# Kernel tuning notes

Hardware: AMD Instinct MI355X
Metric: run time of the kernel (lower is better)

The kernel has to match this reference:

```python
import jax, jax.numpy as jnp
import numpy as np

N_NODES = 50000
N_EDGES = 800000
IN_DIM = 128
HEADS = 4
CH = 64
NEG_SLOPE = 0.2


def _gat_conv(x, src, dst, W, a_src, a_dst, bias):
    """PyG-style GATConv (self-loops already appended to src/dst).
    x: [N, F_in], W: [F_in, H*C], a_src/a_dst: [H, C], bias: [H*C]."""
    n = x.shape[0]
    h = (x @ W).reshape(n, HEADS, CH)                      # [N, H, C]
    alpha_s = (h * a_src).sum(-1)                          # [N, H]
    alpha_d = (h * a_dst).sum(-1)                          # [N, H]
    e = jax.nn.leaky_relu(alpha_s[src] + alpha_d[dst], NEG_SLOPE)  # [E, H]
    m = jax.ops.segment_max(e, dst, num_segments=n)        # segment softmax over dst
    e = jnp.exp(e - m[dst])
    denom = jax.ops.segment_sum(e, dst, num_segments=n)
    alpha = e / (denom[dst] + 1e-16)                       # [E, H]
    out = jax.ops.segment_sum(h[src] * alpha[:, :, None], dst, num_segments=n)
    return out.reshape(n, HEADS * CH) + bias               # concat=True


def setup_inputs() -> dict:
    key = jax.random.key(0)
    ks = jax.random.split(key, 10)
    x = jax.random.normal(ks[0], (N_NODES, IN_DIM), dtype=jnp.float32)
    edge_index = jax.random.randint(ks[1], (2, N_EDGES), 0, N_NODES, dtype=jnp.int64)
    s1 = 1.0 / np.sqrt(IN_DIM)
    s2 = 1.0 / np.sqrt(HEADS * CH)
    return {
        "x": x,
        "edge_index": edge_index,
        "W1": jax.random.normal(ks[2], (IN_DIM, HEADS * CH), dtype=jnp.float32) * s1,
        "a_src1": jax.random.normal(ks[3], (HEADS, CH), dtype=jnp.float32) * s1,
        "a_dst1": jax.random.normal(ks[4], (HEADS, CH), dtype=jnp.float32) * s1,
        "b1": jnp.zeros((HEADS * CH,), dtype=jnp.float32),
        "W2": jax.random.normal(ks[5], (HEADS * CH, HEADS * CH), dtype=jnp.float32) * s2,
        "a_src2": jax.random.normal(ks[6], (HEADS, CH), dtype=jnp.float32) * s2,
        "a_dst2": jax.random.normal(ks[7], (HEADS, CH), dtype=jnp.float32) * s2,
        "b2": jnp.zeros((HEADS * CH,), dtype=jnp.float32),
        "fc_w": jax.random.normal(ks[8], (HEADS * CH, 1), dtype=jnp.float32) * s2,
        "fc_b": jnp.zeros((1,), dtype=jnp.float32),
    }


def reference(x, edge_index, W1, a_src1, a_dst1, b1, W2, a_src2, a_dst2, b2, fc_w, fc_b):
    n = x.shape[0]
    loop = jnp.arange(n, dtype=edge_index.dtype)           # PyG GATConv adds self-loops
    src = jnp.concatenate([edge_index[0], loop])
    dst = jnp.concatenate([edge_index[1], loop])
    h = jax.nn.elu(_gat_conv(x, src, dst, W1, a_src1, a_dst1, b1))
    h = jax.nn.elu(_gat_conv(h, src, dst, W2, a_src2, a_dst2, b2))
    return jax.nn.sigmoid(h @ fc_w + fc_b)                 # [N, 1]
```

## Files before the change

### kernel.cpp

```cpp
#include <hip/hip_runtime.h>
#include <hip/hip_bf16.h>

#define N_NODES 50000
#define N_EDGES 800000
#define NCHUNK 256
#define EPC 3125
#define NBUCKET 196
#define SCAN_N 50176
#define SCAN_BLOCKS 196

typedef __attribute__((ext_vector_type(8))) short bf16x8;
typedef __attribute__((ext_vector_type(4))) float f32x4;
typedef __attribute__((ext_vector_type(2))) float f32x2;
typedef unsigned short ushort_t;

__device__ __forceinline__ float bf2f(unsigned short u) {
    union { unsigned u32; float f; } v; v.u32 = (unsigned)u << 16; return v.f;
}
__device__ __forceinline__ unsigned short f2bf(float f) {
    __hip_bfloat16 h = __float2bfloat16(f);
    return *reinterpret_cast<unsigned short*>(&h);
}
__device__ __forceinline__ f32x2 bfpair(unsigned u) {
    union { unsigned a; float f; } lo, hi;
    lo.a = u << 16;
    hi.a = u & 0xFFFF0000u;
    f32x2 r; r.x = lo.f; r.y = hi.f; return r;
}
__device__ __forceinline__ void pkfma(f32x2& d, f32x2 a, f32x2 b) {
    asm("v_pk_fma_f32 %0, %1, %2, %0" : "+v"(d) : "v"(a), "v"(b));
}
__device__ __forceinline__ void gload16(const void* src, void* lds) {
    __builtin_amdgcn_global_load_lds(
        (const __attribute__((address_space(1))) unsigned int*)src,
        (__attribute__((address_space(3))) unsigned int*)lds, 16, 0, 0);
}

__device__ __forceinline__ int detect_is32_block(const unsigned* __restrict__ w,
                                                 int* s_is32, int tid) {
    if (tid == 0) {
        unsigned o = 0;
#pragma unroll
        for (int k = 1; k < 32; k += 2) o |= w[k];
        *s_is32 = (o != 0u);
    }
    __syncthreads();
    return *s_is32;
}

__device__ __forceinline__ int edge_elem(const unsigned* __restrict__ w, int is32, long long idx) {
    return is32 ? (int)w[idx] : (int)w[2 * idx];
}

#define CONV_BLOCKS 6250
#define PREP_W_BLOCKS (CONV_BLOCKS + 128 + 256)
__global__ void __launch_bounds__(256) prep_kernel(const float* __restrict__ x,
                                                   ushort_t* __restrict__ xbf,
                                                   const float* __restrict__ W1,
                                                   ushort_t* __restrict__ W1t,
                                                   const float* __restrict__ W2,
                                                   ushort_t* __restrict__ W2t,
                                                   const unsigned* __restrict__ ew,
                                                   int* __restrict__ chunkHist,
                                                   int* __restrict__ dhist,
                                                   int* __restrict__ dcur) {
    int b = blockIdx.x, t = threadIdx.x;
    if (b < CONV_BLOCKS) {
        if (b == 0 && t < 64) { dhist[t] = 0; dcur[t] = 0; }
        int i = b * 256 + t;
        float4 v = ((const float4*)x)[i];
        ushort4 o;
        o.x = f2bf(v.x); o.y = f2bf(v.y); o.z = f2bf(v.z); o.w = f2bf(v.w);
        ((ushort4*)xbf)[i] = o;
    } else if (b < CONV_BLOCKS + 128) {
        int id = (b - CONV_BLOCKS) * 256 + t;
        int n = id >> 7, k = id & 127;
        W1t[id] = f2bf(W1[k * 256 + n]);
    } else if (b < CONV_BLOCKS + 128 + 256) {
        int id = (b - CONV_BLOCKS - 128) * 256 + t;
        int n = id >> 8, k = id & 255;
        W2t[id] = f2bf(W2[k * 256 + n]);
    } else {
        __shared__ int s_is32;
        __shared__ int hist[NBUCKET];
        int c = b - PREP_W_BLOCKS;
        int is32 = detect_is32_block(ew, &s_is32, t);
        for (int k = t; k < NBUCKET; k += 256) hist[k] = 0;
        __syncthreads();
        long long e0 = (long long)c * EPC;
        for (int k = t; k < EPC; k += 256) {
            int d = edge_elem(ew, is32, (long long)N_EDGES + e0 + k);
            atomicAdd(&hist[d >> 8], 1);
        }
        __syncthreads();
        for (int k = t; k < NBUCKET; k += 256)
            chunkHist[k * NCHUNK + c] = hist[k];
    }
}

__global__ void __launch_bounds__(256) scan1_kernel(const int* __restrict__ in,
                                                    int* __restrict__ excl, int* __restrict__ bsum) {
    __shared__ int s[256];
    int b = blockIdx.x, t = threadIdx.x, i = b * 256 + t;
    int v = in[i];
    s[t] = v;
    __syncthreads();
    for (int off = 1; off < 256; off <<= 1) {
        int y = (t >= off) ? s[t - off] : 0;
        __syncthreads();
        s[t] += y;
        __syncthreads();
    }
    excl[i] = s[t] - v;
    if (t == 255) bsum[b] = s[255];
}

__global__ void __launch_bounds__(256) scan3_kernel(const int* __restrict__ bsum,
                                                    int* __restrict__ excl) {
    __shared__ int sboff;
    int b = blockIdx.x, t = threadIdx.x;
    if (t < 64) {
        int add = 0;
        for (int k = t; k < b; k += 64) add += bsum[k];
#pragma unroll
        for (int off = 32; off; off >>= 1) add += __shfl_down(add, off, 64);
        if (t == 0) sboff = add;
    }
    __syncthreads();
    excl[b * 256 + t] += sboff;
}

__global__ void __launch_bounds__(256) bucket_scatter_kernel(const unsigned* __restrict__ ew,
                                                             const int* __restrict__ chunkOff,
                                                             unsigned* __restrict__ ebuf) {
    __shared__ int s_is32;
    __shared__ int cur[NBUCKET];
    int t = threadIdx.x, b = blockIdx.x;
    int is32 = detect_is32_block(ew, &s_is32, t);
    for (int k = t; k < NBUCKET; k += 256) cur[k] = chunkOff[k * NCHUNK + b];
    __syncthreads();
    long long e0 = (long long)b * EPC;
    for (int k = t; k < EPC; k += 256) {
        long long e = e0 + k;
        unsigned s = (unsigned)edge_elem(ew, is32, e);
        int d = edge_elem(ew, is32, (long long)N_EDGES + e);
        int pos = atomicAdd(&cur[d >> 8], 1);
        ebuf[pos] = s | ((unsigned)d << 16);
    }
}

__global__ void __launch_bounds__(256) bucket_sort_kernel(const unsigned* __restrict__ ebuf,
                                                          const int* __restrict__ chunkOff,
                                                          unsigned* __restrict__ edge_csr,
                                                          int* __restrict__ row_ptr,
                                                          int* __restrict__ dhist) {
    __shared__ int cnt[256];
    __shared__ int s[256];
    __shared__ int dh[64];
    int b = blockIdx.x, t = threadIdx.x;
    int start = chunkOff[b * NCHUNK];
    int end = (b + 1 < NBUCKET) ? chunkOff[(b + 1) * NCHUNK] : N_EDGES;
    cnt[t] = 0;
    if (t < 64) dh[t] = 0;
    __syncthreads();
    for (int e = start + t; e < end; e += 256) {
        int d = (int)(ebuf[e] >> 16);
        atomicAdd(&cnt[d & 255], 1);
    }
    __syncthreads();
    int node = b * 256 + t;
    int mydeg = cnt[t];
    if (node < N_NODES) atomicAdd(&dh[mydeg < 63 ? mydeg : 63], 1);
    s[t] = mydeg;
    __syncthreads();
    for (int off = 1; off < 256; off <<= 1) {
        int y = (t >= off) ? s[t - off] : 0;
        __syncthreads();
        s[t] += y;
        __syncthreads();
    }
    int excl = s[t] - mydeg;
    if (node <= N_NODES) row_ptr[node] = start + excl;
    cnt[t] = start + excl;
    __syncthreads();
    for (int e = start + t; e < end; e += 256) {
        unsigned pk = ebuf[e];
        int pos = atomicAdd(&cnt[(pk >> 16) & 255], 1);
        edge_csr[pos] = pk;
    }
    if (t < 64 && dh[t]) atomicAdd(&dhist[t], dh[t]);
}

__global__ void __launch_bounds__(256) dscatter_kernel(const int* __restrict__ row_ptr,
                                                       const int* __restrict__ dhist,
                                                       int* __restrict__ dcur,
                                                       int* __restrict__ perm) {
    __shared__ int lh[64], lbase[64], sbase[64];
    int t = threadIdx.x, i = blockIdx.x * 256 + t;
    if (t < 64) {
        int v = dhist[t];
        int sum = v;
#pragma unroll
        for (int off = 1; off < 64; off <<= 1) {
            int y = __shfl_up(sum, off, 64);
            if (t >= off) sum += y;
        }
        sbase[t] = sum - v;
        lh[t] = 0;
    }
    __syncthreads();
    int deg = 0;
    if (i < N_NODES) {
        deg = row_ptr[i + 1] - row_ptr[i];
        if (deg > 63) deg = 63;
        atomicAdd(&lh[deg], 1);
    }
    __syncthreads();
    if (t < 64) {
        lbase[t] = lh[t] ? (sbase[t] + atomicAdd(&dcur[t], lh[t])) : 0;
        lh[t] = 0;
    }
    __syncthreads();
    if (i < N_NODES) {
        int rank = atomicAdd(&lh[deg], 1);
        perm[lbase[deg] + rank] = i;
    }
}

template <int K>
__global__ void __launch_bounds__(256) mfma_gemm_kernel(const ushort_t* __restrict__ A,
                                                        const ushort_t* __restrict__ Wt,
                                                        void* __restrict__ Cv, int M,
                                                        const float* __restrict__ a_src,
                                                        const float* __restrict__ a_dst,
                                                        float* __restrict__ alpha_s,
                                                        float* __restrict__ alpha_d) {
    constexpr int CPR = K / 8;
    constexpr int NT = K / 64;
    __shared__ ushort_t Bs[64 * K];
    __shared__ ushort_t As[2][64 * 64];
    __shared__ float ps[64][2], pd[64][2];

    int tid = threadIdx.x;
    int wave = tid >> 6, lane = tid & 63;
    int l15 = lane & 15, l4 = lane >> 4;
    int wr = wave >> 1, wc = wave & 1;
    int colblock = blockIdx.x;
    int rowblock = blockIdx.y;

    for (int base = 0; base < 64 * CPR; base += 256) {
        int p = base + wave * 64 + lane;
        int row = p / CPR;
        int cs = p % CPR;
        int c = cs ^ (row & 7);
        const ushort_t* src = Wt + (long long)(colblock * 64 + row) * K + c * 8;
        void* dst = ((char*)Bs) + (base + wave * 64) * 16;
        gload16(src, dst);
    }
    {
        int r = lane >> 3, cs = lane & 7;
        int c = cs ^ r;
#pragma unroll
        for (int q = 0; q < 2; ++q) {
            int lrow = wave * 16 + q * 8;
            int grow = rowblock * 64 + lrow + r;
            if (grow >= M) grow = M - 1;
            const ushort_t* src = A + (long long)grow * K + c * 8;
            void* dst = ((char*)&As[0][0]) + lrow * 128;
            gload16(src, dst);
        }
    }
    __syncthreads();

    f32x4 acc[2][2] = {};
#pragma unroll
    for (int t = 0; t < NT; ++t) {
        if (t + 1 < NT) {
            int r = lane >> 3, cs = lane & 7;
            int c = cs ^ r;
#pragma unroll
            for (int q = 0; q < 2; ++q) {
                int lrow = wave * 16 + q * 8;
                int grow = rowblock * 64 + lrow + r;
                if (grow >= M) grow = M - 1;
                const ushort_t* src = A + (long long)grow * K + (t + 1) * 64 + c * 8;
                void* dst = ((char*)&As[(t + 1) & 1][0]) + lrow * 128;
                gload16(src, dst);
            }
        }
        const ushort_t* At = &As[t & 1][0];
#pragma unroll
        for (int w = 0; w < 2; ++w) {
            bf16x8 a[2], b[2];
#pragma unroll
            for (int mi = 0; mi < 2; ++mi) {
                int row = wr * 32 + mi * 16 + l15;
                int slot = (w * 4 + l4) ^ (l15 & 7);
                a[mi] = *(const bf16x8*)&At[row * 64 + slot * 8];
            }
#pragma unroll
            for (int ni = 0; ni < 2; ++ni) {
                int brow = wc * 32 + ni * 16 + l15;
                int slot = (t * 8 + w * 4 + l4) ^ (l15 & 7);
                b[ni] = *(const bf16x8*)&Bs[brow * CPR * 8 + slot * 8];
            }
#pragma unroll
            for (int mi = 0; mi < 2; ++mi)
#pragma unroll
                for (int ni = 0; ni < 2; ++ni)
                    acc[mi][ni] = __builtin_amdgcn_mfma_f32_16x16x32_bf16(a[mi], b[ni],
                                                                          acc[mi][ni], 0, 0, 0);
        }
        __syncthreads();
    }

    {
        float as0 = a_src[colblock * 64 + wc * 32 + l15];
        float as1 = a_src[colblock * 64 + wc * 32 + 16 + l15];
        float ad0 = a_dst[colblock * 64 + wc * 32 + l15];
        float ad1 = a_dst[colblock * 64 + wc * 32 + 16 + l15];
#pragma unroll
        for (int mi = 0; mi < 2; ++mi)
#pragma unroll
            for (int q = 0; q < 4; ++q) {
                float sv = acc[mi][0][q] * as0 + acc[mi][1][q] * as1;
                float dv = acc[mi][0][q] * ad0 + acc[mi][1][q] * ad1;
#pragma unroll
                for (int w = 1; w < 16; w <<= 1) {
                    sv += __shfl_xor(sv, w, 64);
                    dv += __shfl_xor(dv, w, 64);
                }
                if (l15 == 0) {
                    int row = wr * 32 + mi * 16 + l4 * 4 + q;
                    ps[row][wc] = sv;
                    pd[row][wc] = dv;
                }
            }
    }

    ushort_t* ep = ((ushort_t*)&As[0][0]) + wave * 1280;
#pragma unroll
    for (int mi = 0; mi < 2; ++mi)
#pragma unroll
        for (int ni = 0; ni < 2; ++ni)
#pragma unroll
            for (int q = 0; q < 4; ++q) {
                int row = mi * 16 + l4 * 4 + q;
                int col = ni * 16 + l15;
                ep[row * 40 + col] = f2bf(acc[mi][ni][q]);
            }
    __syncthreads();
#pragma unroll
    for (int j = 0; j < 2; ++j) {
        int p = lane * 2 + j;
        int row = p >> 2, seg = p & 3;
        uint4 v = *(const uint4*)&ep[row * 40 + seg * 8];
        int grow = rowblock * 64 + wr * 32 + row;
        int gcol = colblock * 64 + wc * 32 + seg * 8;
        if (grow < M) {
            f32x2 f01 = bfpair(v.x), f23 = bfpair(v.y);
            f32x2 f45 = bfpair(v.z), f67 = bfpair(v.w);
            int d0 = 0, d1 = 0;
            d0 = __builtin_amdgcn_cvt_pk_fp8_f32(f01.x, f01.y, d0, false);
            d0 = __builtin_amdgcn_cvt_pk_fp8_f32(f23.x, f23.y, d0, true);
            d1 = __builtin_amdgcn_cvt_pk_fp8_f32(f45.x, f45.y, d1, false);
            d1 = __builtin_amdgcn_cvt_pk_fp8_f32(f67.x, f67.y, d1, true);
            uint2 o; o.x = (unsigned)d0; o.y = (unsigned)d1;
            *(uint2*)((char*)Cv + (long long)grow * 256 + gcol) = o;
        }
    }
    if (tid < 64) {
        int ga = rowblock * 64 + tid;
        if (ga < M) {
            alpha_s[ga * 4 + colblock] = ps[tid][0] + ps[tid][1];
            alpha_d[ga * 4 + colblock] = pd[tid][0] + pd[tid][1];
        }
    }
}

template <int U>
__device__ __forceinline__ void agg_batch(int p, const unsigned* __restrict__ edge_csr,
                                          const float* __restrict__ alpha_s,
                                          const char* __restrict__ gb, unsigned loff,
                                          int l15, int hd, float ad, float& wsum,
                                          f32x2& acc01, f32x2& acc23) {
    int j[U]; unsigned hh[U];
#pragma unroll
    for (int u = 0; u < U; ++u) j[u] = (int)(edge_csr[p + u] & 0xFFFFu);
#pragma unroll
    for (int u = 0; u < U; ++u)
        hh[u] = *(const unsigned*)(gb + (((unsigned)j[u] << 8) | loff));
    int myj = (int)(edge_csr[p + (l15 & (U - 1))] & 0xFFFFu);
    float e = alpha_s[myj * 4 + hd] + ad;
    e = e > 0.f ? e : 0.2f * e;
    float wt_mine = __expf(e);
    int sbase = hd << 4;
#pragma unroll
    for (int u = 0; u < U; ++u) {
        float wt = __shfl(wt_mine, sbase | u, 64);
        wsum += wt;
        f32x2 wp; wp.x = wt; wp.y = wt;
        pkfma(acc01, wp, __builtin_amdgcn_cvt_pk_f32_fp8(hh[u], false));
        pkfma(acc23, wp, __builtin_amdgcn_cvt_pk_f32_fp8(hh[u], true));
    }
}

template <int LAYER>
__global__ void __launch_bounds__(256) aggregate_kernel(
    const void* __restrict__ gv, const float* __restrict__ alpha_s,
    const float* __restrict__ alpha_d, const int* __restrict__ row_ptr,
    const unsigned* __restrict__ edge_csr, const int* __restrict__ perm,
    const float* __restrict__ bias, ushort_t* __restrict__ out_bf,
    const float* __restrict__ fc_w, const float* __restrict__ fc_b,
    float* __restrict__ final_out) {
    int wave = threadIdx.x >> 6;
    int lane = threadIdx.x & 63;
    int i = __builtin_amdgcn_readfirstlane(perm[blockIdx.x * 4 + wave]);
    int hd = lane >> 4;
    int l15 = lane & 15;
    const char* gb = (const char*)gv;
    unsigned loff = (unsigned)(lane << 2);

    float ad = alpha_d[i * 4 + hd];
    float e0 = alpha_s[i * 4 + hd] + ad;
    e0 = e0 > 0.f ? e0 : 0.2f * e0;
    float w0 = __expf(e0);
    f32x2 acc01 = {0.f, 0.f}, acc23 = {0.f, 0.f};
    {
        unsigned sv = *(const unsigned*)(gb + (((unsigned)i << 8) | loff));
        f32x2 wp0; wp0.x = w0; wp0.y = w0;
        pkfma(acc01, wp0, __builtin_amdgcn_cvt_pk_f32_fp8(sv, false));
        pkfma(acc23, wp0, __builtin_amdgcn_cvt_pk_f32_fp8(sv, true));
    }
    float wsum = w0;

    int p = __builtin_amdgcn_readfirstlane(row_ptr[i]);
    int p1 = __builtin_amdgcn_readfirstlane(row_ptr[i + 1]);
    for (; p + 16 <= p1; p += 16)
        agg_batch<16>(p, edge_csr, alpha_s, gb, loff, l15, hd, ad, wsum, acc01, acc23);
    for (; p + 8 <= p1; p += 8)
        agg_batch<8>(p, edge_csr, alpha_s, gb, loff, l15, hd, ad, wsum, acc01, acc23);
    for (; p + 4 <= p1; p += 4)
        agg_batch<4>(p, edge_csr, alpha_s, gb, loff, l15, hd, ad, wsum, acc01, acc23);
    for (; p < p1; ++p)
        agg_batch<1>(p, edge_csr, alpha_s, gb, loff, l15, hd, ad, wsum, acc01, acc23);

    float inv = 1.f / (wsum + 1e-16f);
    int c = lane * 4;
    float4 b4 = *(const float4*)&bias[c];
    float o0 = acc01.x * inv + b4.x;
    float o1 = acc01.y * inv + b4.y;
    float o2 = acc23.x * inv + b4.z;
    float o3 = acc23.y * inv + b4.w;
    o0 = o0 > 0.f ? o0 : __expf(o0) - 1.f;
    o1 = o1 > 0.f ? o1 : __expf(o1) - 1.f;
    o2 = o2 > 0.f ? o2 : __expf(o2) - 1.f;
    o3 = o3 > 0.f ? o3 : __expf(o3) - 1.f;
    if (LAYER == 1) {
        ushort4 o;
        o.x = f2bf(o0); o.y = f2bf(o1); o.z = f2bf(o2); o.w = f2bf(o3);
        ((ushort4*)out_bf)[(long long)i * 64 + lane] = o;
    } else {
        float4 fw = *(const float4*)&fc_w[c];
        float dot = o0 * fw.x + o1 * fw.y + o2 * fw.z + o3 * fw.w;
#pragma unroll
        for (int off = 32; off; off >>= 1) dot += __shfl_down(dot, off, 64);
        if (lane == 0) final_out[i] = 1.f / (1.f + __expf(-(dot + fc_b[0])));
    }
}

extern "C" void kernel_launch(void* const* d_in, const int* in_sizes, int n_in,
                              void* d_out, int out_size, void* d_ws, size_t ws_size,
                              hipStream_t stream) {
    const float* x   = (const float*)d_in[0];
    const unsigned* ei = (const unsigned*)d_in[1];
    const float* W1  = (const float*)d_in[2];
    const float* as1 = (const float*)d_in[3];
    const float* ad1 = (const float*)d_in[4];
    const float* b1  = (const float*)d_in[5];
    const float* W2  = (const float*)d_in[6];
    const float* as2 = (const float*)d_in[7];
    const float* ad2 = (const float*)d_in[8];
    const float* b2  = (const float*)d_in[9];
    const float* fcw = (const float*)d_in[10];
    const float* fcb = (const float*)d_in[11];

    char* ws = (char*)d_ws;
    void* g1f8         = (void*)(ws + 0);
    void* g2f8         = (void*)(ws + 12800000);
    ushort_t* hactbf   = (ushort_t*)(ws + 25600000);
    ushort_t* xbf      = (ushort_t*)(ws + 51200000);
    ushort_t* W1t      = (ushort_t*)(ws + 64000000);
    ushort_t* W2t      = (ushort_t*)(ws + 64100000);
    float* asv         = (float*)(ws + 64300000);
    float* adv         = (float*)(ws + 65100000);
    int* row_ptr       = (int*)(ws + 65900000);
    int* chunkHist     = (int*)(ws + 66110000);
    int* chunkOff      = (int*)(ws + 66320000);
    unsigned* ebuf     = (unsigned*)(ws + 66530000);
    unsigned* edge_csr = (unsigned*)(ws + 69730000);
    int* perm          = (int*)(ws + 72930000);
    int* bsum          = (int*)(ws + 73130000);
    int* dhist         = (int*)(ws + 73132048);
    int* dcur          = (int*)(ws + 73132304);

    prep_kernel<<<PREP_W_BLOCKS + NCHUNK, 256, 0, stream>>>(x, xbf, W1, W1t, W2, W2t,
                                                            ei, chunkHist, dhist, dcur);
    scan1_kernel<<<SCAN_BLOCKS, 256, 0, stream>>>(chunkHist, chunkOff, bsum);
    scan3_kernel<<<SCAN_BLOCKS, 256, 0, stream>>>(bsum, chunkOff);
    bucket_scatter_kernel<<<NCHUNK, 256, 0, stream>>>(ei, chunkOff, ebuf);
    bucket_sort_kernel<<<NBUCKET, 256, 0, stream>>>(ebuf, chunkOff, edge_csr, row_ptr, dhist);
    dscatter_kernel<<<SCAN_BLOCKS, 256, 0, stream>>>(row_ptr, dhist, dcur, perm);

    mfma_gemm_kernel<128><<<dim3(4, (N_NODES + 63) / 64), 256, 0, stream>>>(
        xbf, W1t, g1f8, N_NODES, as1, ad1, asv, adv);
    aggregate_kernel<1><<<N_NODES / 4, 256, 0, stream>>>(g1f8, asv, adv, row_ptr, edge_csr, perm,
                                                         b1, hactbf, nullptr, nullptr, nullptr);
    mfma_gemm_kernel<256><<<dim3(4, (N_NODES + 63) / 64), 256, 0, stream>>>(
        hactbf, W2t, g2f8, N_NODES, as2, ad2, asv, adv);
    aggregate_kernel<2><<<N_NODES / 4, 256, 0, stream>>>(g2f8, asv, adv, row_ptr, edge_csr, perm,
                                                         b2, nullptr, fcw, fcb, (float*)d_out);
}
```

Baseline: 174.7 us.

## Fuse CSR build stages into one cooperative kernel with grid syncs

Replaces the six small CSR-construction launches (histogram, two scan passes, bucket scatter, bucket sort, degree scatter) with one cooperative kernel of 256 blocks that uses grid-wide syncs between phases. The edge histogram moves out of prep_kernel into this kernel, and the second-level scan becomes a single-block scan into a new boff buffer. The aim is to remove launch overhead and inter-kernel gaps on a latency-bound preprocessing chain. In exchange it adds grid.sync barriers and depends on all 256 blocks being co-resident.

```diff
diff --git a/kernel.cpp b/kernel.cpp
--- a/kernel.cpp
+++ b/kernel.cpp
@@ -1,13 +1,14 @@
 #include <hip/hip_runtime.h>
 #include <hip/hip_bf16.h>
+#include <hip/hip_cooperative_groups.h>
+
+namespace cg = cooperative_groups;
 
 #define N_NODES 50000
 #define N_EDGES 800000
 #define NCHUNK 256
 #define EPC 3125
 #define NBUCKET 196
-#define SCAN_N 50176
-#define SCAN_BLOCKS 196
 
 typedef __attribute__((ext_vector_type(8))) short bf16x8;
 typedef __attribute__((ext_vector_type(4))) float f32x4;
@@ -59,14 +60,9 @@
                                                    const float* __restrict__ W1,
                                                    ushort_t* __restrict__ W1t,
                                                    const float* __restrict__ W2,
-                                                   ushort_t* __restrict__ W2t,
-                                                   const unsigned* __restrict__ ew,
-                                                   int* __restrict__ chunkHist,
-                                                   int* __restrict__ dhist,
-                                                   int* __restrict__ dcur) {
+                                                   ushort_t* __restrict__ W2t) {
     int b = blockIdx.x, t = threadIdx.x;
     if (b < CONV_BLOCKS) {
-        if (b == 0 && t < 64) { dhist[t] = 0; dcur[t] = 0; }
         int i = b * 256 + t;
         float4 v = ((const float4*)x)[i];
         ushort4 o;
@@ -76,154 +72,152 @@
         int id = (b - CONV_BLOCKS) * 256 + t;
         int n = id >> 7, k = id & 127;
         W1t[id] = f2bf(W1[k * 256 + n]);
-    } else if (b < CONV_BLOCKS + 128 + 256) {
+    } else {
         int id = (b - CONV_BLOCKS - 128) * 256 + t;
         int n = id >> 8, k = id & 255;
         W2t[id] = f2bf(W2[k * 256 + n]);
-    } else {
-        __shared__ int s_is32;
-        __shared__ int hist[NBUCKET];
-        int c = b - PREP_W_BLOCKS;
-        int is32 = detect_is32_block(ew, &s_is32, t);
-        for (int k = t; k < NBUCKET; k += 256) hist[k] = 0;
-        __syncthreads();
-        long long e0 = (long long)c * EPC;
+    }
+}
+
+__global__ void __launch_bounds__(256) csr_build_kernel(
+    const unsigned* __restrict__ ew, int* __restrict__ chunkHist,
+    int* __restrict__ chunkOff, int* __restrict__ bsum, int* __restrict__ boff,
+    unsigned* __restrict__ ebuf, unsigned* __restrict__ edge_csr,
+    int* __restrict__ row_ptr, int* __restrict__ dhist, int* __restrict__ dcur,
+    int* __restrict__ perm) {
+    cg::grid_group grid = cg::this_grid();
+    int b = blockIdx.x, t = threadIdx.x;
+    __shared__ int s_is32;
+    __shared__ int sh[256];
+    __shared__ int sh2[256];
+    __shared__ int d64a[64], d64b[64], d64c[64];
+
+    int is32 = detect_is32_block(ew, &s_is32, t);
+
+    if (b == 0 && t < 64) { dhist[t] = 0; dcur[t] = 0; }
+    for (int k = t; k < NBUCKET; k += 256) sh[k] = 0;
+    __syncthreads();
+    {
+        long long e0 = (long long)b * EPC;
         for (int k = t; k < EPC; k += 256) {
             int d = edge_elem(ew, is32, (long long)N_EDGES + e0 + k);
-            atomicAdd(&hist[d >> 8], 1);
-        }
-        __syncthreads();
-        for (int k = t; k < NBUCKET; k += 256)
-            chunkHist[k * NCHUNK + c] = hist[k];
-    }
-}
-
-__global__ void __launch_bounds__(256) scan1_kernel(const int* __restrict__ in,
-                                                    int* __restrict__ excl, int* __restrict__ bsum) {
-    __shared__ int s[256];
-    int b = blockIdx.x, t = threadIdx.x, i = b * 256 + t;
-    int v = in[i];
-    s[t] = v;
+            atomicAdd(&sh[d >> 8], 1);
+        }
+    }
     __syncthreads();
-    for (int off = 1; off < 256; off <<= 1) {
-        int y = (t >= off) ? s[t - off] : 0;
-        __syncthreads();
-        s[t] += y;
-        __syncthreads();
-    }
-    excl[i] = s[t] - v;
-    if (t == 255) bsum[b] = s[255];
-}
-
-__global__ void __launch_bounds__(256) scan3_kernel(const int* __restrict__ bsum,
-                                                    int* __restrict__ excl) {
-    __shared__ int sboff;
-    int b = blockIdx.x, t = threadIdx.x;
-    if (t < 64) {
-        int add = 0;
-        for (int k = t; k < b; k += 64) add += bsum[k];
-#pragma unroll
-        for (int off = 32; off; off >>= 1) add += __shfl_down(add, off, 64);
-        if (t == 0) sboff = add;
-    }
+    for (int k = t; k < NBUCKET; k += 256) chunkHist[k * NCHUNK + b] = sh[k];
+    grid.sync();
+
+    if (b < NBUCKET) {
+        int i = b * 256 + t;
+        int v = chunkHist[i];
+        sh[t] = v;
+        __syncthreads();
+        for (int off = 1; off < 256; off <<= 1) {
+            int y = (t >= off) ? sh[t - off] : 0;
+            __syncthreads();
+            sh[t] += y;
+            __syncthreads();
+        }
+        chunkOff[i] = sh[t] - v;
+        if (t == 255) bsum[b] = sh[255];
+    }
+    grid.sync();
+
+    if (b == 0) {
+        int v = (t < NBUCKET) ? bsum[t] : 0;
+        sh[t] = v;
+        __syncthreads();
+        for (int off = 1; off < 256; off <<= 1) {
+            int y = (t >= off) ? sh[t - off] : 0;
+            __syncthreads();
+            sh[t] += y;
+            __syncthreads();
+        }
+        if (t < NBUCKET) boff[t] = sh[t] - v;
+    }
+    grid.sync();
+
+    if (b < NBUCKET) chunkOff[b * 256 + t] += boff[b];
+    grid.sync();
+
+    for (int k = t; k < NBUCKET; k += 256) sh[k] = chunkOff[k * NCHUNK + b];
     __syncthreads();
-    excl[b * 256 + t] += sboff;
-}
-
-__global__ void __launch_bounds__(256) bucket_scatter_kernel(const unsigned* __restrict__ ew,
-                                                             const int* __restrict__ chunkOff,
-                                                             unsigned* __restrict__ ebuf) {
-    __shared__ int s_is32;
-    __shared__ int cur[NBUCKET];
-    int t = threadIdx.x, b = blockIdx.x;
-    int is32 = detect_is32_block(ew, &s_is32, t);
-    for (int k = t; k < NBUCKET; k += 256) cur[k] = chunkOff[k * NCHUNK + b];
-    __syncthreads();
-    long long e0 = (long long)b * EPC;
-    for (int k = t; k < EPC; k += 256) {
-        long long e = e0 + k;
-        unsigned s = (unsigned)edge_elem(ew, is32, e);
-        int d = edge_elem(ew, is32, (long long)N_EDGES + e);
-        int pos = atomicAdd(&cur[d >> 8], 1);
-        ebuf[pos] = s | ((unsigned)d << 16);
-    }
-}
-
-__global__ void __launch_bounds__(256) bucket_sort_kernel(const unsigned* __restrict__ ebuf,
-                                                          const int* __restrict__ chunkOff,
-                                                          unsigned* __restrict__ edge_csr,
-                                                          int* __restrict__ row_ptr,
-                                                          int* __restrict__ dhist) {
-    __shared__ int cnt[256];
-    __shared__ int s[256];
-    __shared__ int dh[64];
-    int b = blockIdx.x, t = threadIdx.x;
-    int start = chunkOff[b * NCHUNK];
-    int end = (b + 1 < NBUCKET) ? chunkOff[(b + 1) * NCHUNK] : N_EDGES;
-    cnt[t] = 0;
-    if (t < 64) dh[t] = 0;
-    __syncthreads();
-    for (int e = start + t; e < end; e += 256) {
-        int d = (int)(ebuf[e] >> 16);
-        atomicAdd(&cnt[d & 255], 1);
-    }
-    __syncthreads();
-    int node = b * 256 + t;
-    int mydeg = cnt[t];
-    if (node < N_NODES) atomicAdd(&dh[mydeg < 63 ? mydeg : 63], 1);
-    s[t] = mydeg;
-    __syncthreads();
-    for (int off = 1; off < 256; off <<= 1) {
-        int y = (t >= off) ? s[t - off] : 0;
-        __syncthreads();
-        s[t] += y;
-        __syncthreads();
-    }
-    int excl = s[t] - mydeg;
-    if (node <= N_NODES) row_ptr[node] = start + excl;
-    cnt[t] = start + excl;
-    __syncthreads();
-    for (int e = start + t; e < end; e += 256) {
-        unsigned pk = ebuf[e];
-        int pos = atomicAdd(&cnt[(pk >> 16) & 255], 1);
-        edge_csr[pos] = pk;
-    }
-    if (t < 64 && dh[t]) atomicAdd(&dhist[t], dh[t]);
-}
-
-__global__ void __launch_bounds__(256) dscatter_kernel(const int* __restrict__ row_ptr,
-                                                       const int* __restrict__ dhist,
-                                                       int* __restrict__ dcur,
-                                                       int* __restrict__ perm) {
-    __shared__ int lh[64], lbase[64], sbase[64];
-    int t = threadIdx.x, i = blockIdx.x * 256 + t;
-    if (t < 64) {
-        int v = dhist[t];
-        int sum = v;
-#pragma unroll
-        for (int off = 1; off < 64; off <<= 1) {
-            int y = __shfl_up(sum, off, 64);
-            if (t >= off) sum += y;
-        }
-        sbase[t] = sum - v;
-        lh[t] = 0;
-    }
-    __syncthreads();
-    int deg = 0;
-    if (i < N_NODES) {
-        deg = row_ptr[i + 1] - row_ptr[i];
-        if (deg > 63) deg = 63;
-        atomicAdd(&lh[deg], 1);
-    }
-    __syncthreads();
-    if (t < 64) {
-        lbase[t] = lh[t] ? (sbase[t] + atomicAdd(&dcur[t], lh[t])) : 0;
-        lh[t] = 0;
-    }
-    __syncthreads();
-    if (i < N_NODES) {
-        int rank = atomicAdd(&lh[deg], 1);
-        perm[lbase[deg] + rank] = i;
+    {
+        long long e0 = (long long)b * EPC;
+        for (int k = t; k < EPC; k += 256) {
+            long long e = e0 + k;
+            unsigned s = (unsigned)edge_elem(ew, is32, e);
+            int d = edge_elem(ew, is32, (long long)N_EDGES + e);
+            int pos = atomicAdd(&sh[d >> 8], 1);
+            ebuf[pos] = s | ((unsigned)d << 16);
+        }
+    }
+    grid.sync();
+
+    if (b < NBUCKET) {
+        int start = chunkOff[b * NCHUNK];
+        int end = (b + 1 < NBUCKET) ? chunkOff[(b + 1) * NCHUNK] : N_EDGES;
+        sh[t] = 0;
+        if (t < 64) d64a[t] = 0;
+        __syncthreads();
+        for (int e = start + t; e < end; e += 256)
+            atomicAdd(&sh[(int)(ebuf[e] >> 16) & 255], 1);
+        __syncthreads();
+        int node = b * 256 + t;
+        int mydeg = sh[t];
+        if (node < N_NODES) atomicAdd(&d64a[mydeg < 63 ? mydeg : 63], 1);
+        sh2[t] = mydeg;
+        __syncthreads();
+        for (int off = 1; off < 256; off <<= 1) {
+            int y = (t >= off) ? sh2[t - off] : 0;
+            __syncthreads();
+            sh2[t] += y;
+            __syncthreads();
+        }
+        int excl = sh2[t] - mydeg;
+        if (node <= N_NODES) row_ptr[node] = start + excl;
+        sh[t] = start + excl;
+        __syncthreads();
+        for (int e = start + t; e < end; e += 256) {
+            unsigned pk = ebuf[e];
+            int pos = atomicAdd(&sh[(pk >> 16) & 255], 1);
+            edge_csr[pos] = pk;
+        }
+        if (t < 64 && d64a[t]) atomicAdd(&dhist[t], d64a[t]);
+    }
+    grid.sync();
+
+    if (b < NBUCKET) {
+        int i = b * 256 + t;
+        if (t < 64) {
+            int v = dhist[t];
+            int sum = v;
+#pragma unroll
+            for (int off = 1; off < 64; off <<= 1) {
+                int y = __shfl_up(sum, off, 64);
+                if (t >= off) sum += y;
+            }
+            d64b[t] = sum - v;
+            d64a[t] = 0;
+        }
+        __syncthreads();
+        int deg = 0;
+        if (i < N_NODES) {
+            deg = row_ptr[i + 1] - row_ptr[i];
+            if (deg > 63) deg = 63;
+            atomicAdd(&d64a[deg], 1);
+        }
+        __syncthreads();
+        if (t < 64) {
+            d64c[t] = d64a[t] ? (d64b[t] + atomicAdd(&dcur[t], d64a[t])) : 0;
+            d64a[t] = 0;
+        }
+        __syncthreads();
+        if (i < N_NODES) {
+            int rank = atomicAdd(&d64a[deg], 1);
+            perm[d64c[deg] + rank] = i;
+        }
     }
 }
 
@@ -501,16 +495,19 @@
     unsigned* edge_csr = (unsigned*)(ws + 69730000);
     int* perm          = (int*)(ws + 72930000);
     int* bsum          = (int*)(ws + 73130000);
+    int* boff          = (int*)(ws + 73131024);
     int* dhist         = (int*)(ws + 73132048);
     int* dcur          = (int*)(ws + 73132304);
 
-    prep_kernel<<<PREP_W_BLOCKS + NCHUNK, 256, 0, stream>>>(x, xbf, W1, W1t, W2, W2t,
-                                                            ei, chunkHist, dhist, dcur);
-    scan1_kernel<<<SCAN_BLOCKS, 256, 0, stream>>>(chunkHist, chunkOff, bsum);
-    scan3_kernel<<<SCAN_BLOCKS, 256, 0, stream>>>(bsum, chunkOff);
-    bucket_scatter_kernel<<<NCHUNK, 256, 0, stream>>>(ei, chunkOff, ebuf);
-    bucket_sort_kernel<<<NBUCKET, 256, 0, stream>>>(ebuf, chunkOff, edge_csr, row_ptr, dhist);
-    dscatter_kernel<<<SCAN_BLOCKS, 256, 0, stream>>>(row_ptr, dhist, dcur, perm);
+    prep_kernel<<<PREP_W_BLOCKS, 256, 0, stream>>>(x, xbf, W1, W1t, W2, W2t);
+
+    {
+        void* cargs[] = {(void*)&ei, (void*)&chunkHist, (void*)&chunkOff, (void*)&bsum,
+                         (void*)&boff, (void*)&ebuf, (void*)&edge_csr, (void*)&row_ptr,
+                         (void*)&dhist, (void*)&dcur, (void*)&perm};
+        hipLaunchCooperativeKernel((const void*)csr_build_kernel, dim3(NCHUNK), dim3(256),
+                                   cargs, 0, stream);
+    }
 
     mfma_gemm_kernel<128><<<dim3(4, (N_NODES + 63) / 64), 256, 0, stream>>>(
         xbf, W1t, g1f8, N_NODES, as1, ad1, asv, adv);
```

Measured after the change: 356.9 us. 2.04x slower.
